# Kernel optimization log

Hardware: AMD Instinct MI355X
Metric: run time of the kernel (lower is better)

## Reference

```python
import jax, jax.numpy as jnp
import numpy as np

# dims: P points, CIN in_channels (z), COUT out_channels (v), T n_terms (a/b),
# N spatial index extent (i and j share it since pair_features is reused), X summed axis
P, CIN, COUT, T, N, X = 64, 16, 16, 4, 32, 64
EINSUM = 'pzijx,paix,pbjx,azv,bzv->pvij'


def setup_inputs() -> dict:
    key = jax.random.key(0)
    k0, k1, k2, k3 = jax.random.split(key, 4)
    features_weighted = jax.random.normal(k0, (P, CIN, N, N, X), dtype=jnp.float32)
    pair_features = jax.random.normal(k1, (P, T, N, X), dtype=jnp.float32)
    # kaiming_uniform fan_in (relu): bound = sqrt(6 / fan_in); emulate scale with normal init
    scale = np.float32(np.sqrt(2.0 / CIN))
    w0 = jax.random.normal(k2, (T, CIN, COUT), dtype=jnp.float32) * scale
    w1 = jax.random.normal(k3, (T, CIN, COUT), dtype=jnp.float32) * scale
    bias = jnp.zeros((COUT, 1, 1), dtype=jnp.float32)  # (out_channels,) + (1,)*(n_dim-1)
    return {
        'features_weighted': features_weighted,
        'pair_features': pair_features,
        'w0': w0,
        'w1': w1,
        'bias': bias,
    }


def reference(features_weighted, pair_features, w0, w1, bias):
    # multi-tensor contraction: pair_features enters twice (as 'paix' and 'pbjx')
    feats = jnp.einsum(EINSUM, features_weighted, pair_features, pair_features, w0, w1)
    # feats: (P, COUT, N, N); bias (COUT,1,1) broadcasts over the two spatial dims
    return jax.nn.relu(feats + bias)
```

## Files before the change

### kernel.cpp

```cpp
#include <hip/hip_runtime.h>

#define NP    64
#define NCIN  16
#define NCOUT 16
#define NT    4
#define NN    32
#define NX    64

typedef __attribute__((ext_vector_type(8))) __bf16 bf16x8;
typedef __attribute__((ext_vector_type(4))) float  f32x4;

__device__ __forceinline__ unsigned pk_bf16(float lo, float hi) {
    unsigned ulo = __float_as_uint(lo) + 0x8000u;
    unsigned uhi = __float_as_uint(hi) + 0x8000u;
    return __builtin_amdgcn_perm(uhi, ulo, 0x07060302u);
}

__global__ __launch_bounds__(256) void higher_point_kernel(
    const float* __restrict__ FW,
    const float* __restrict__ PF,
    const float* __restrict__ W0,
    const float* __restrict__ W1,
    const float* __restrict__ BIAS,
    float* __restrict__ OUT)
{
    __shared__ float pf_lds[NT * NN * NX];

    const int bx   = blockIdx.x;
    const int p    = bx >> 5;
    const int i    = bx & 31;
    const int tid  = threadIdx.x;
    const int lane = tid & 63;
    const int wave = tid >> 6;

    {
        const float4* pf_g = (const float4*)(PF + p * (NT * NN * NX));
        float4* pf_s = (float4*)pf_lds;
        #pragma unroll
        for (int k = 0; k < 8; ++k) pf_s[tid + k * 256] = pf_g[tid + k * 256];
    }
    __syncthreads();

    const int c = lane & 15;
    const int q = lane >> 4;
    const int aIdx = c >> 2;
    const int bIdx = c & 3;

    float ww[4][16];
    #pragma unroll
    for (int r = 0; r < 4; ++r) {
        const int z = q * 4 + r;
        const float4* w0r = (const float4*)(W0 + (aIdx * NCIN + z) * NCOUT);
        const float4* w1r = (const float4*)(W1 + (bIdx * NCIN + z) * NCOUT);
        #pragma unroll
        for (int t4i = 0; t4i < 4; ++t4i) {
            float4 x0 = w0r[t4i], x1 = w1r[t4i];
            ww[r][t4i * 4 + 0] = x0.x * x1.x;
            ww[r][t4i * 4 + 1] = x0.y * x1.y;
            ww[r][t4i * 4 + 2] = x0.z * x1.z;
            ww[r][t4i * 4 + 3] = x0.w * x1.w;
        }
    }

    const float biasv = BIAS[lane >> 2];

    float pfi0[8], pfi1[8];
    {
        const float* base = pf_lds + (aIdx * NN + i) * NX + q * 8;
        #pragma unroll
        for (int e = 0; e < 8; ++e) { pfi0[e] = base[e]; pfi1[e] = base[32 + e]; }
    }

    const float* fw_row = FW + ((p * NCIN + c) * (NN * NN) + i * NN) * NX + q * 8;

    const int j0 = wave * 8;

    float4 nf0a, nf0b, nf1a, nf1b;
    {
        const float* rb = fw_row + j0 * NX;
        nf0a = ((const float4*)rb)[0];
        nf0b = ((const float4*)rb)[1];
        nf1a = ((const float4*)(rb + 32))[0];
        nf1b = ((const float4*)(rb + 32))[1];
    }

    for (int jj = 0; jj < 8; ++jj) {
        const int j = j0 + jj;
        float4 f0a = nf0a, f0b = nf0b, f1a = nf1a, f1b = nf1b;
        if (jj < 7) {
            const float* rb = fw_row + (j + 1) * NX;
            nf0a = ((const float4*)rb)[0];
            nf0b = ((const float4*)rb)[1];
            nf1a = ((const float4*)(rb + 32))[0];
            nf1b = ((const float4*)(rb + 32))[1];
        }

        float pfj0[8], pfj1[8];
        {
            const float* base = pf_lds + (bIdx * NN + j) * NX + q * 8;
            #pragma unroll
            for (int e = 0; e < 8; ++e) { pfj0[e] = base[e]; pfj1[e] = base[32 + e]; }
        }

        union { unsigned u[4]; bf16x8 v; } A0, A1, B0, B1;
        A0.u[0] = pk_bf16(f0a.x, f0a.y); A0.u[1] = pk_bf16(f0a.z, f0a.w);
        A0.u[2] = pk_bf16(f0b.x, f0b.y); A0.u[3] = pk_bf16(f0b.z, f0b.w);
        A1.u[0] = pk_bf16(f1a.x, f1a.y); A1.u[1] = pk_bf16(f1a.z, f1a.w);
        A1.u[2] = pk_bf16(f1b.x, f1b.y); A1.u[3] = pk_bf16(f1b.z, f1b.w);

        float r0[8], r1[8];
        #pragma unroll
        for (int e = 0; e < 8; ++e) { r0[e] = pfi0[e] * pfj0[e]; r1[e] = pfi1[e] * pfj1[e]; }
        B0.u[0] = pk_bf16(r0[0], r0[1]); B0.u[1] = pk_bf16(r0[2], r0[3]);
        B0.u[2] = pk_bf16(r0[4], r0[5]); B0.u[3] = pk_bf16(r0[6], r0[7]);
        B1.u[0] = pk_bf16(r1[0], r1[1]); B1.u[1] = pk_bf16(r1[2], r1[3]);
        B1.u[2] = pk_bf16(r1[4], r1[5]); B1.u[3] = pk_bf16(r1[6], r1[7]);

        f32x4 acc = {0.f, 0.f, 0.f, 0.f};
        acc = __builtin_amdgcn_mfma_f32_16x16x32_bf16(A0.v, B0.v, acc, 0, 0, 0);
        acc = __builtin_amdgcn_mfma_f32_16x16x32_bf16(A1.v, B1.v, acc, 0, 0, 0);

        float partial[16];
        #pragma unroll
        for (int v = 0; v < 16; ++v)
            partial[v] = acc[0] * ww[0][v] + acc[1] * ww[1][v]
                       + acc[2] * ww[2][v] + acc[3] * ww[3][v];

        const bool b5 = (lane & 32) != 0;
        const bool b4 = (lane & 16) != 0;
        const bool b3 = (lane & 8)  != 0;
        const bool b2 = (lane & 4)  != 0;

        float t8[8];
        #pragma unroll
        for (int k = 0; k < 8; ++k) {
            float mine   = b5 ? partial[k + 8] : partial[k];
            float theirs = b5 ? partial[k]     : partial[k + 8];
            t8[k] = mine + __shfl_xor(theirs, 32, 64);
        }
        float t4[4];
        #pragma unroll
        for (int k = 0; k < 4; ++k) {
            float mine   = b4 ? t8[k + 4] : t8[k];
            float theirs = b4 ? t8[k]     : t8[k + 4];
            t4[k] = mine + __shfl_xor(theirs, 16, 64);
        }
        float t2[2];
        #pragma unroll
        for (int k = 0; k < 2; ++k) {
            float mine   = b3 ? t4[k + 2] : t4[k];
            float theirs = b3 ? t4[k]     : t4[k + 2];
            t2[k] = mine + __shfl_xor(theirs, 8, 64);
        }
        float mine1   = b2 ? t2[1] : t2[0];
        float theirs1 = b2 ? t2[0] : t2[1];
        float s = mine1 + __shfl_xor(theirs1, 4, 64);
        s += __shfl_xor(s, 2, 64);
        s += __shfl_xor(s, 1, 64);

        if ((lane & 3) == 0) {
            float rv = s + biasv;
            OUT[((p * NCOUT + (lane >> 2)) * NN + i) * NN + j] = rv > 0.f ? rv : 0.f;
        }
    }
}

extern "C" void kernel_launch(void* const* d_in, const int* in_sizes, int n_in,
                              void* d_out, int out_size, void* d_ws, size_t ws_size,
                              hipStream_t stream) {
    const float* FW   = (const float*)d_in[0];
    const float* PF   = (const float*)d_in[1];
    const float* W0   = (const float*)d_in[2];
    const float* W1   = (const float*)d_in[3];
    const float* BIAS = (const float*)d_in[4];
    float* OUT = (float*)d_out;

    hipLaunchKernelGGL(higher_point_kernel, dim3(NP * NN), dim3(256), 0, stream,
                       FW, PF, W0, W1, BIAS, OUT);
}
```

Before: 371.6 us.

## Replace shuffle-based weight contraction with a second MFMA stage via LDS

The per-j scalar weight contraction followed by a long cross-lane shuffle reduction is replaced by a second stage. Each wave stores its first-stage MFMA results as bf16 in LDS, then runs eight MFMAs against precomputed bf16 W0*W1 fragments and writes 16 outputs per lane group. Blocks now cover two i values with 16 j each. The shared pair_features LDS staging is dropped in favour of direct global loads, and launch bounds request higher occupancy. This removes heavy VALU and shuffle work, but adds bf16 rounding of intermediates and uncached repeated pf_j global reads.

```diff
diff --git a/kernel.cpp b/kernel.cpp
--- a/kernel.cpp
+++ b/kernel.cpp
@@ -16,7 +16,10 @@
     return __builtin_amdgcn_perm(uhi, ulo, 0x07060302u);
 }
 
-__global__ __launch_bounds__(256) void higher_point_kernel(
+#define QROW_DW  140
+#define QWAVE_DW (16 * QROW_DW)
+
+__global__ __launch_bounds__(256, 4) void higher_point_kernel(
     const float* __restrict__ FW,
     const float* __restrict__ PF,
     const float* __restrict__ W0,
@@ -24,83 +27,76 @@
     const float* __restrict__ BIAS,
     float* __restrict__ OUT)
 {
-    __shared__ float pf_lds[NT * NN * NX];
+    __shared__ unsigned qlds[4 * QWAVE_DW];
 
-    const int bx   = blockIdx.x;
-    const int p    = bx >> 5;
-    const int i    = bx & 31;
-    const int tid  = threadIdx.x;
-    const int lane = tid & 63;
-    const int wave = tid >> 6;
+    const int bx    = blockIdx.x;
+    const int p     = bx >> 4;
+    const int ipair = bx & 15;
+    const int tid   = threadIdx.x;
+    const int lane  = tid & 63;
+    const int wave  = tid >> 6;
+    const int i     = ipair * 2 + (wave >> 1);
+    const int j0    = (wave & 1) * 16;
 
-    {
-        const float4* pf_g = (const float4*)(PF + p * (NT * NN * NX));
-        float4* pf_s = (float4*)pf_lds;
-        #pragma unroll
-        for (int k = 0; k < 8; ++k) pf_s[tid + k * 256] = pf_g[tid + k * 256];
-    }
-    __syncthreads();
-
-    const int c = lane & 15;
-    const int q = lane >> 4;
+    const int c    = lane & 15;
+    const int q    = lane >> 4;
     const int aIdx = c >> 2;
     const int bIdx = c & 3;
 
-    float ww[4][16];
+    unsigned* qbase = qlds + wave * QWAVE_DW;
+
+    bf16x8 wwfrag[8];
     #pragma unroll
-    for (int r = 0; r < 4; ++r) {
-        const int z = q * 4 + r;
-        const float4* w0r = (const float4*)(W0 + (aIdx * NCIN + z) * NCOUT);
-        const float4* w1r = (const float4*)(W1 + (bIdx * NCIN + z) * NCOUT);
+    for (int m = 0; m < 8; ++m) {
+        union { unsigned u[4]; bf16x8 v; } W;
         #pragma unroll
-        for (int t4i = 0; t4i < 4; ++t4i) {
-            float4 x0 = w0r[t4i], x1 = w1r[t4i];
-            ww[r][t4i * 4 + 0] = x0.x * x1.x;
-            ww[r][t4i * 4 + 1] = x0.y * x1.y;
-            ww[r][t4i * 4 + 2] = x0.z * x1.z;
-            ww[r][t4i * 4 + 3] = x0.w * x1.w;
+        for (int e2 = 0; e2 < 4; ++e2) {
+            const int k0 = m * 32 + q * 8 + e2 * 2;
+            const int k1 = k0 + 1;
+            float v0 = W0[((k0 >> 6) * NCIN + (k0 & 15)) * NCOUT + c] *
+                       W1[(((k0 >> 4) & 3) * NCIN + (k0 & 15)) * NCOUT + c];
+            float v1 = W0[((k1 >> 6) * NCIN + (k1 & 15)) * NCOUT + c] *
+                       W1[(((k1 >> 4) & 3) * NCIN + (k1 & 15)) * NCOUT + c];
+            W.u[e2] = pk_bf16(v0, v1);
         }
+        wwfrag[m] = W.v;
     }
-
-    const float biasv = BIAS[lane >> 2];
 
     float pfi0[8], pfi1[8];
     {
-        const float* base = pf_lds + (aIdx * NN + i) * NX + q * 8;
-        #pragma unroll
-        for (int e = 0; e < 8; ++e) { pfi0[e] = base[e]; pfi1[e] = base[32 + e]; }
+        const float* pib = PF + ((p * NT + aIdx) * NN + i) * NX + q * 8;
+        float4 a0 = ((const float4*)pib)[0];
+        float4 a1 = ((const float4*)pib)[1];
+        float4 b0 = ((const float4*)(pib + 32))[0];
+        float4 b1 = ((const float4*)(pib + 32))[1];
+        pfi0[0]=a0.x; pfi0[1]=a0.y; pfi0[2]=a0.z; pfi0[3]=a0.w;
+        pfi0[4]=a1.x; pfi0[5]=a1.y; pfi0[6]=a1.z; pfi0[7]=a1.w;
+        pfi1[0]=b0.x; pfi1[1]=b0.y; pfi1[2]=b0.z; pfi1[3]=b0.w;
+        pfi1[4]=b1.x; pfi1[5]=b1.y; pfi1[6]=b1.z; pfi1[7]=b1.w;
     }
 
-    const float* fw_row = FW + ((p * NCIN + c) * (NN * NN) + i * NN) * NX + q * 8;
+    const float* fw_base = FW + (((p * NCIN + c) * NN + i) * NN + j0) * NX + q * 8;
+    const float* pf_jb   = PF + ((p * NT + bIdx) * NN + j0) * NX + q * 8;
 
-    const int j0 = wave * 8;
+    float4 nf0a = ((const float4*)fw_base)[0];
+    float4 nf0b = ((const float4*)fw_base)[1];
+    float4 nf1a = ((const float4*)(fw_base + 32))[0];
+    float4 nf1b = ((const float4*)(fw_base + 32))[1];
 
-    float4 nf0a, nf0b, nf1a, nf1b;
-    {
-        const float* rb = fw_row + j0 * NX;
-        nf0a = ((const float4*)rb)[0];
-        nf0b = ((const float4*)rb)[1];
-        nf1a = ((const float4*)(rb + 32))[0];
-        nf1b = ((const float4*)(rb + 32))[1];
-    }
-
-    for (int jj = 0; jj < 8; ++jj) {
-        const int j = j0 + jj;
+    for (int jj = 0; jj < 16; ++jj) {
         float4 f0a = nf0a, f0b = nf0b, f1a = nf1a, f1b = nf1b;
-        if (jj < 7) {
-            const float* rb = fw_row + (j + 1) * NX;
-            nf0a = ((const float4*)rb)[0];
-            nf0b = ((const float4*)rb)[1];
-            nf1a = ((const float4*)(rb + 32))[0];
-            nf1b = ((const float4*)(rb + 32))[1];
+        if (jj < 15) {
+            const float* nb = fw_base + (jj + 1) * NX;
+            nf0a = ((const float4*)nb)[0];
+            nf0b = ((const float4*)nb)[1];
+            nf1a = ((const float4*)(nb + 32))[0];
+            nf1b = ((const float4*)(nb + 32))[1];
         }
-
-        float pfj0[8], pfj1[8];
-        {
-            const float* base = pf_lds + (bIdx * NN + j) * NX + q * 8;
-            #pragma unroll
-            for (int e = 0; e < 8; ++e) { pfj0[e] = base[e]; pfj1[e] = base[32 + e]; }
-        }
+        const float* pj = pf_jb + jj * NX;
+        float4 pj0a = ((const float4*)pj)[0];
+        float4 pj0b = ((const float4*)pj)[1];
+        float4 pj1a = ((const float4*)(pj + 32))[0];
+        float4 pj1b = ((const float4*)(pj + 32))[1];
 
         union { unsigned u[4]; bf16x8 v; } A0, A1, B0, B1;
         A0.u[0] = pk_bf16(f0a.x, f0a.y); A0.u[1] = pk_bf16(f0a.z, f0a.w);
@@ -108,60 +104,40 @@
         A1.u[0] = pk_bf16(f1a.x, f1a.y); A1.u[1] = pk_bf16(f1a.z, f1a.w);
         A1.u[2] = pk_bf16(f1b.x, f1b.y); A1.u[3] = pk_bf16(f1b.z, f1b.w);
 
-        float r0[8], r1[8];
-        #pragma unroll
-        for (int e = 0; e < 8; ++e) { r0[e] = pfi0[e] * pfj0[e]; r1[e] = pfi1[e] * pfj1[e]; }
-        B0.u[0] = pk_bf16(r0[0], r0[1]); B0.u[1] = pk_bf16(r0[2], r0[3]);
-        B0.u[2] = pk_bf16(r0[4], r0[5]); B0.u[3] = pk_bf16(r0[6], r0[7]);
-        B1.u[0] = pk_bf16(r1[0], r1[1]); B1.u[1] = pk_bf16(r1[2], r1[3]);
-        B1.u[2] = pk_bf16(r1[4], r1[5]); B1.u[3] = pk_bf16(r1[6], r1[7]);
+        B0.u[0] = pk_bf16(pfi0[0] * pj0a.x, pfi0[1] * pj0a.y);
+        B0.u[1] = pk_bf16(pfi0[2] * pj0a.z, pfi0[3] * pj0a.w);
+        B0.u[2] = pk_bf16(pfi0[4] * pj0b.x, pfi0[5] * pj0b.y);
+        B0.u[3] = pk_bf16(pfi0[6] * pj0b.z, pfi0[7] * pj0b.w);
+        B1.u[0] = pk_bf16(pfi1[0] * pj1a.x, pfi1[1] * pj1a.y);
+        B1.u[1] = pk_bf16(pfi1[2] * pj1a.z, pfi1[3] * pj1a.w);
+        B1.u[2] = pk_bf16(pfi1[4] * pj1b.x, pfi1[5] * pj1b.y);
+        B1.u[3] = pk_bf16(pfi1[6] * pj1b.z, pfi1[7] * pj1b.w);
 
         f32x4 acc = {0.f, 0.f, 0.f, 0.f};
         acc = __builtin_amdgcn_mfma_f32_16x16x32_bf16(A0.v, B0.v, acc, 0, 0, 0);
         acc = __builtin_amdgcn_mfma_f32_16x16x32_bf16(A1.v, B1.v, acc, 0, 0, 0);
 
-        float partial[16];
-        #pragma unroll
-        for (int v = 0; v < 16; ++v)
-            partial[v] = acc[0] * ww[0][v] + acc[1] * ww[1][v]
-                       + acc[2] * ww[2][v] + acc[3] * ww[3][v];
+        uint2 qw;
+        qw.x = pk_bf16(acc[0], acc[1]);
+        qw.y = pk_bf16(acc[2], acc[3]);
+        *(uint2*)(qbase + jj * QROW_DW + c * 8 + q * 2) = qw;
+    }
 
-        const bool b5 = (lane & 32) != 0;
-        const bool b4 = (lane & 16) != 0;
-        const bool b3 = (lane & 8)  != 0;
-        const bool b2 = (lane & 4)  != 0;
+    __syncthreads();
 
-        float t8[8];
-        #pragma unroll
-        for (int k = 0; k < 8; ++k) {
-            float mine   = b5 ? partial[k + 8] : partial[k];
-            float theirs = b5 ? partial[k]     : partial[k + 8];
-            t8[k] = mine + __shfl_xor(theirs, 32, 64);
-        }
-        float t4[4];
-        #pragma unroll
-        for (int k = 0; k < 4; ++k) {
-            float mine   = b4 ? t8[k + 4] : t8[k];
-            float theirs = b4 ? t8[k]     : t8[k + 4];
-            t4[k] = mine + __shfl_xor(theirs, 16, 64);
-        }
-        float t2[2];
-        #pragma unroll
-        for (int k = 0; k < 2; ++k) {
-            float mine   = b3 ? t4[k + 2] : t4[k];
-            float theirs = b3 ? t4[k]     : t4[k + 2];
-            t2[k] = mine + __shfl_xor(theirs, 8, 64);
-        }
-        float mine1   = b2 ? t2[1] : t2[0];
-        float theirs1 = b2 ? t2[0] : t2[1];
-        float s = mine1 + __shfl_xor(theirs1, 4, 64);
-        s += __shfl_xor(s, 2, 64);
-        s += __shfl_xor(s, 1, 64);
+    f32x4 oacc = {0.f, 0.f, 0.f, 0.f};
+    #pragma unroll
+    for (int m = 0; m < 8; ++m) {
+        union { uint4 u4; bf16x8 v; } B;
+        B.u4 = *(const uint4*)(qbase + c * QROW_DW + m * 16 + q * 4);
+        oacc = __builtin_amdgcn_mfma_f32_16x16x32_bf16(wwfrag[m], B.v, oacc, 0, 0, 0);
+    }
 
-        if ((lane & 3) == 0) {
-            float rv = s + biasv;
-            OUT[((p * NCOUT + (lane >> 2)) * NN + i) * NN + j] = rv > 0.f ? rv : 0.f;
-        }
+    #pragma unroll
+    for (int r = 0; r < 4; ++r) {
+        const int v = q * 4 + r;
+        float val = oacc[r] + BIAS[v];
+        OUT[((p * NCOUT + v) * NN + i) * NN + j0 + c] = val > 0.f ? val : 0.f;
     }
 }
 
@@ -175,6 +151,6 @@
     const float* BIAS = (const float*)d_in[4];
     float* OUT = (float*)d_out;
 
-    hipLaunchKernelGGL(higher_point_kernel, dim3(NP * NN), dim3(256), 0, stream,
+    hipLaunchKernelGGL(higher_point_kernel, dim3(NP * NN / 2), dim3(256), 0, stream,
                        FW, PF, W0, W1, BIAS, OUT);
 }
```

After: 375.7 us. No clear change (+1.1%).
